# Optimization experiments

Measured on AMD Instinct MI355X. Metric: run time of the kernel, lower is better.

The kernel has to match this reference:

```python
import jax, jax.numpy as jnp
import numpy as np

B, NW, NS, SL = 32, 500, 50, 40
EMB, HID, VOCAB, E = 300, 150, 50000, 563200
N = B * (NW + NS)
MAXPOS = 512


def _sinusoid(n_pos, d):
    pos = np.arange(n_pos)[:, None].astype(np.float64)
    i = np.arange(d)[None, :]
    ang = pos / np.power(10000.0, 2 * (i // 2) / d)
    tab = np.zeros((n_pos, d))
    tab[:, 0::2] = np.sin(ang[:, 0::2])
    tab[:, 1::2] = np.cos(ang[:, 1::2])
    tab[0] = 0.0  # padding_idx=0
    return jnp.asarray(tab, dtype=jnp.float32)

_POS_TAB = _sinusoid(MAXPOS + 1, EMB)


def setup_inputs():
    keys = iter(jax.random.split(jax.random.key(0), 48))
    def nrm(shape, s=0.05):
        return jax.random.normal(next(keys), shape, dtype=jnp.float32) * s
    inp = {}
    inp["x"] = jax.random.randint(next(keys), (B, NW), 0, VOCAB, dtype=jnp.int32)
    inp["sent_x"] = jax.random.randint(next(keys), (B, NS, SL), 0, VOCAB, dtype=jnp.int32)
    inp["edge_index"] = jax.random.randint(next(keys), (2, E), 0, N, dtype=jnp.int32)
    inp["embed_table"] = nrm((VOCAB, EMB)).at[0].set(0.0)  # padding_idx=0
    for h in range(2, 8):
        inp["conv_w%d" % h] = nrm((50, 1, h, EMB))
        inp["conv_b%d" % h] = nrm((50,))
    inp["cnn_proj_w"] = nrm((HID, EMB)); inp["cnn_proj_b"] = nrm((HID,))
    inp["lstm_w_ih_l0"] = nrm((2, 4 * HID, HID)); inp["lstm_w_hh_l0"] = nrm((2, 4 * HID, HID))
    inp["lstm_b_ih_l0"] = nrm((2, 4 * HID)); inp["lstm_b_hh_l0"] = nrm((2, 4 * HID))
    inp["lstm_w_ih_l1"] = nrm((2, 4 * HID, 2 * HID)); inp["lstm_w_hh_l1"] = nrm((2, 4 * HID, HID))
    inp["lstm_b_ih_l1"] = nrm((2, 4 * HID)); inp["lstm_b_hh_l1"] = nrm((2, 4 * HID))
    inp["lstm_proj_w"] = nrm((HID, 2 * HID)); inp["lstm_proj_b"] = nrm((HID,))
    inp["gc0_w"] = nrm((HID, EMB)); inp["gc0_b"] = nrm((HID,))
    inp["gc1_w"] = nrm((HID, HID)); inp["gc1_b"] = nrm((HID,))
    inp["gc2_w"] = nrm((HID, HID)); inp["gc2_b"] = nrm((HID,))
    return inp


def _forward(x, sent_x, edge_index, embed_table, conv_ws, conv_bs,
             cnn_proj_w, cnn_proj_b, w_ih0, w_hh0, b_ih0, b_hh0,
             w_ih1, w_hh1, b_ih1, b_hh1, lstm_proj_w, lstm_proj_b,
             gc0_w, gc0_b, gc1_w, gc1_b, gc2_w, gc2_b):
    Bsz, S, L = sent_x.shape
    Nn = Bsz * S
    emb_words = embed_table[x]                                   # [B, NW, EMB]
    tok = embed_table[sent_x].reshape(Nn, L, EMB)                # [Nn, L, EMB]
    sentlen = (sent_x != 0).sum(-1).reshape(Nn)                  # token count per sentence
    a = jnp.arange(L)
    input_pos = jnp.where(a[None, :] < sentlen[:, None], a[None, :] + 1, 0)
    enc = tok + _POS_TAB[input_pos]
    # CNN ngram features: conv heights 2..7, full-width kernels == windowed matmuls
    feats = []
    for w, b in zip(conv_ws, conv_bs):
        h = w.shape[2]
        acc = b + sum(jnp.einsum('nld,od->nlo', enc[:, k:L - h + 1 + k, :], w[:, 0, k, :]) for k in range(h))
        feats.append(jnp.max(jax.nn.relu(acc), axis=1))          # [Nn, 50]
    ngram = jnp.concatenate(feats, axis=1)                        # [Nn, 300]
    snode_pos = jnp.tile(jnp.arange(S), Bsz)
    cnn_feat = ((ngram + _POS_TAB[snode_pos]) @ cnn_proj_w.T + cnn_proj_b).reshape(Bsz, S, HID)
    glen = (sent_x[:, :, 0] != 0).sum(-1)                         # valid sentence count per graph

    def lstm_dir(xs, w_ih, w_hh, bias):
        def step(carry, xt):
            hh, cc = carry
            g = xt @ w_ih.T + hh @ w_hh.T + bias
            i, f, gg, o = jnp.split(g, 4, axis=-1)
            cc = jax.nn.sigmoid(f) * cc + jax.nn.sigmoid(i) * jnp.tanh(gg)
            hh = jax.nn.sigmoid(o) * jnp.tanh(cc)
            return (hh, cc), hh
        z = jnp.zeros((xs.shape[0], HID), xs.dtype)
        _, hs = jax.lax.scan(step, (z, z), jnp.swapaxes(xs, 0, 1))
        return jnp.swapaxes(hs, 0, 1)

    def rev_within(xs):
        # reverse only the first glen[b] steps (packed-sequence semantics)
        T = xs.shape[1]; t = jnp.arange(T)
        idx = jnp.where(t[None, :] < glen[:, None], glen[:, None] - 1 - t[None, :], t[None, :])
        return jnp.take_along_axis(xs, idx[:, :, None], axis=1)

    def bidir(xs, w_ih, w_hh, b_i, b_h):
        f = lstm_dir(xs, w_ih[0], w_hh[0], b_i[0] + b_h[0])
        r = rev_within(lstm_dir(rev_within(xs), w_ih[1], w_hh[1], b_i[1] + b_h[1]))
        return jnp.concatenate([f, r], axis=-1)

    h1 = bidir(cnn_feat, w_ih0, w_hh0, b_ih0, b_hh0)
    h2 = bidir(h1, w_ih1, w_hh1, b_ih1, b_hh1)
    mask = (jnp.arange(S)[None, :] < glen[:, None]).astype(h2.dtype)[:, :, None]
    lstm_feat = (h2 * mask) @ lstm_proj_w.T + lstm_proj_b
    sent_out = jnp.concatenate([cnn_feat, lstm_feat], axis=-1)    # [B, S, 300]
    nodes = jnp.concatenate([emb_words, sent_out], axis=1)        # [B, NW+S, 300]
    nodes = (nodes @ gc0_w.T + gc0_b).reshape(-1, HID)            # [N, 150]
    Nt = nodes.shape[0]
    loop = jnp.arange(Nt, dtype=edge_index.dtype)
    src = jnp.concatenate([edge_index[0], loop])                  # add self-loops
    dst = jnp.concatenate([edge_index[1], loop])
    deg = jax.ops.segment_sum(jnp.ones(src.shape[0], nodes.dtype), dst, num_segments=Nt)
    dis = jnp.where(deg > 0, jax.lax.rsqrt(deg), 0.0)
    norm = (dis[src] * dis[dst])[:, None]

    def gcn(xin, w, bias):
        xw = xin @ w.T
        return jax.ops.segment_sum(xw[src] * norm, dst, num_segments=Nt) + bias

    h = jax.nn.elu(gcn(nodes, gc1_w, gc1_b))
    # F.dropout with training=False -> identity
    return gcn(h, gc2_w, gc2_b), emb_words


def reference(x, sent_x, edge_index, embed_table, conv_w2, conv_b2, conv_w3, conv_b3,
              conv_w4, conv_b4, conv_w5, conv_b5, conv_w6, conv_b6, conv_w7, conv_b7,
              cnn_proj_w, cnn_proj_b, lstm_w_ih_l0, lstm_w_hh_l0, lstm_b_ih_l0, lstm_b_hh_l0,
              lstm_w_ih_l1, lstm_w_hh_l1, lstm_b_ih_l1, lstm_b_hh_l1, lstm_proj_w, lstm_proj_b,
              gc0_w, gc0_b, gc1_w, gc1_b, gc2_w, gc2_b):
    conv_ws = [conv_w2, conv_w3, conv_w4, conv_w5, conv_w6, conv_w7]
    conv_bs = [conv_b2, conv_b3, conv_b4, conv_b5, conv_b6, conv_b7]
    return _forward(x, sent_x, edge_index, embed_table, conv_ws, conv_bs,
                    cnn_proj_w, cnn_proj_b, lstm_w_ih_l0, lstm_w_hh_l0, lstm_b_ih_l0, lstm_b_hh_l0,
                    lstm_w_ih_l1, lstm_w_hh_l1, lstm_b_ih_l1, lstm_b_hh_l1, lstm_proj_w, lstm_proj_b,
                    gc0_w, gc0_b, gc1_w, gc1_b, gc2_w, gc2_b)
```

## Files before the change

kernel.cpp:

```cpp
#include <hip/hip_runtime.h>
#include <stdint.h>
#include <math.h>

#define EDGES 563200
#define NNODES 17600
#define OUT0SZ 2640000
#define MROWS 64000
#define MPAD  64016
#define KSTRIDE 2112

typedef _Float16 h2 __attribute__((ext_vector_type(2)));
typedef _Float16 h4 __attribute__((ext_vector_type(4)));
typedef _Float16 v8h __attribute__((ext_vector_type(8)));
typedef float v4f __attribute__((ext_vector_type(4)));

__device__ __forceinline__ float sigm(float x){ return 1.f / (1.f + expf(-x)); }

__device__ __forceinline__ float fdot2_(h2 a, h2 b, float c){
#if __has_builtin(__builtin_amdgcn_fdot2)
  return __builtin_amdgcn_fdot2(a, b, c, false);
#else
  return c + (float)a.x * (float)b.x + (float)a.y * (float)b.y;
#endif
}

__device__ __forceinline__ void stage16(const char* g, char* lds_base, int lane){
#if __has_builtin(__builtin_amdgcn_global_load_lds)
  __builtin_amdgcn_global_load_lds(
      (const __attribute__((address_space(1))) void*)g,
      (__attribute__((address_space(3))) void*)lds_base, 16, 0, 0);
#else
  uint4 v = *(const uint4*)g;
  *(uint4*)(lds_base + lane * 16) = v;
#endif
}

__global__ __launch_bounds__(1024)
void gcnk_prep2(const int* __restrict__ sx, int* __restrict__ sentlen,
                int* __restrict__ glen_g, int* __restrict__ rowmap){
  __shared__ int sg[32];
  int tid = threadIdx.x;
  for (int i = tid; i < 1600; i += 1024){
    int c = 0;
    for (int j = 0; j < 40; j++) c += (sx[i * 40 + j] != 0);
    sentlen[i] = c;
  }
  if (tid < 32){
    int c = 0;
    for (int s = 0; s < 50; s++) c += (sx[tid * 2000 + s * 40] != 0);
    glen_g[tid] = c; sg[tid] = c;
  }
  __syncthreads();
  for (int i = tid; i < 1600; i += 1024){
    int b = i / 50, t = i - b * 50, g = sg[b];
    rowmap[i] = b * 50 + ((t < g) ? (g - 1 - t) : t);
  }
}

__global__ __launch_bounds__(256)
void gcnk_mergedprep(float* __restrict__ pos,
                     const float* w2, const float* w3, const float* w4,
                     const float* w5, const float* w6, const float* w7,
                     const float* c2, const float* c3, const float* c4,
                     const float* c5, const float* c6, const float* c7,
                     _Float16* __restrict__ Bp, float* __restrict__ bias_p,
                     const float* __restrict__ whh0, _Float16* __restrict__ wpad0,
                     const float* __restrict__ whh1, _Float16* __restrict__ wpad1,
                     unsigned int* __restrict__ ngram_u, unsigned int* __restrict__ ecnt_u,
                     const int* __restrict__ x, const float* __restrict__ tab,
                     float4* __restrict__ out1){
  int blk = blockIdx.x, tid = threadIdx.x;
  if (blk < 602){
    int idx = blk * 256 + tid;
    if (idx >= 513 * 300) return;
    int p = idx / 300, i = idx - p * 300;
    float v = 0.f;
    if (p != 0){
      double expo = (double)(2 * (i / 2)) / 300.0;
      double ang = (double)p / pow(10000.0, expo);
      v = (float)((i & 1) ? cos(ang) : sin(ang));
    }
    pos[idx] = v;
  } else if (blk < 3242){
    int idx = (blk - 602) * 256 + tid;
    if (idx < 2 * 160 * KSTRIDE){
      int n = idx / KSTRIDE, kk = idx - n * KSTRIDE;
      int g = n / 160, c = n - g * 160;
      _Float16 v = (_Float16)0.f;
      if (c < 150){
        int H = 3 * g + 2 + c / 50, o = c % 50;
        if (kk < 300 * H){
          const float* w;
          switch (H){ case 2: w = w2; break; case 3: w = w3; break;
                      case 4: w = w4; break; case 5: w = w5; break;
                      case 6: w = w6; break; default: w = w7; break; }
          v = (_Float16)w[o * 300 * H + kk];
        }
      }
      Bp[idx] = v;
    }
    if (idx < 320){
      int g = idx / 160, c = idx - g * 160;
      float bv = 0.f;
      if (c < 150){
        int H = 3 * g + 2 + c / 50, o = c % 50;
        const float* cbp;
        switch (H){ case 2: cbp = c2; break; case 3: cbp = c3; break;
                    case 4: cbp = c4; break; case 5: cbp = c5; break;
                    case 6: cbp = c6; break; default: cbp = c7; break; }
        bv = cbp[o];
      }
      bias_p[idx] = bv;
    }
  } else if (blk < 3955){
    int idx = (blk - 3242) * 256 + tid;
    if (idx >= 1200 * 152) return;
    int row = idx / 152, col = idx - row * 152;
    wpad0[idx] = (col < 150) ? (_Float16)whh0[row * 150 + col] : (_Float16)0.f;
  } else if (blk < 4668){
    int idx = (blk - 3955) * 256 + tid;
    if (idx >= 1200 * 152) return;
    int row = idx / 152, col = idx - row * 152;
    wpad1[idx] = (col < 150) ? (_Float16)whh1[row * 150 + col] : (_Float16)0.f;
  } else if (blk < 6543){
    int idx = (blk - 4668) * 256 + tid;
    if (idx < 1600 * 300) ngram_u[idx] = 0u;
  } else if (blk < 6612){
    int idx = (blk - 6543) * 256 + tid;
    if (idx < NNODES) ecnt_u[idx] = 0u;
  } else {
    int idx = (blk - 6612) * 256 + tid;
    if (idx >= 16000 * 75) return;
    int row = idx / 75, q = idx - row * 75;
    const float4* t = (const float4*)tab;
    out1[idx] = t[x[row] * 75 + q];
  }
}

__global__ void gcnk_ench(const int* __restrict__ sx, const float* __restrict__ tab,
                          const float* __restrict__ pos, const int* __restrict__ sentlen,
                          _Float16* __restrict__ ench){
  int idx = blockIdx.x * 256 + threadIdx.x;
  if (idx >= MPAD * 75) return;
  int row = idx / 75, q = idx - row * 75;
  int d = q * 4;
  h4 o; o[0] = (_Float16)0.f; o[1] = (_Float16)0.f; o[2] = (_Float16)0.f; o[3] = (_Float16)0.f;
  if (row < MROWS){
    int n = row / 40, l = row - n * 40;
    int tok = sx[n * 40 + l];
    int p = (l < sentlen[n]) ? (l + 1) : 0;
    float4 a = *(const float4*)(tab + (size_t)tok * 300 + d);
    float4 b = *(const float4*)(pos + (size_t)p * 300 + d);
    o[0] = (_Float16)(a.x + b.x); o[1] = (_Float16)(a.y + b.y);
    o[2] = (_Float16)(a.z + b.z); o[3] = (_Float16)(a.w + b.w);
  }
  *(h4*)(ench + (size_t)row * 300 + d) = o;
}

__global__ __launch_bounds__(256)
void gcnk_convmfma(const _Float16* __restrict__ A, const _Float16* __restrict__ Bp,
                   const float* __restrict__ bias_p, unsigned int* __restrict__ ngram_u){
  __shared__ __align__(1024) char smem[36864];
  _Float16* Asm = (_Float16*)smem;
  _Float16* Bsm = (_Float16*)(smem + 16384);
  float* Cs = (float*)smem;
  const int tid = threadIdx.x;
  const int m0 = blockIdx.x * 128;
  const int grp = blockIdx.y;
  const char* Abase = (const char*)A;
  const char* Bbase = (const char*)(Bp + (size_t)grp * 160 * KSTRIDE);
  const int kmax = grp ? 2112 : 1216;
  const int w = tid >> 6, lane = tid & 63;
  const int wm = (w >> 1) * 64, wn = (w & 1) * 80;
  const int fm = lane & 15, fq = lane >> 4;
  const int lrow = lane >> 3;
  const int loff = (((lane & 7) ^ lrow) << 4);

  v4f acc[4][5] = {};

  for (int kc = 0; kc < kmax; kc += 64){
    #pragma unroll
    for (int ii = 0; ii < 4; ii++){
      int i = w * 4 + ii;
      const char* g = Abase + (size_t)(m0 + i * 8 + lrow) * 600 + kc * 2 + loff;
      stage16(g, (char*)Asm + i * 1024, lane);
    }
    #pragma unroll
    for (int jj = 0; jj < 5; jj++){
      int j = w * 5 + jj;
      const char* g = Bbase + (size_t)(j * 8 + lrow) * (KSTRIDE * 2) + kc * 2 + loff;
      stage16(g, (char*)Bsm + j * 1024, lane);
    }
    __syncthreads();
    #pragma unroll
    for (int ks = 0; ks < 2; ks++){
      const int axor = (ks * 64 + fq * 16) ^ ((fm & 7) << 4);
      v8h af[4], bf[5];
      #pragma unroll
      for (int mt = 0; mt < 4; mt++)
        af[mt] = *(const v8h*)((const char*)Asm + (wm + mt * 16 + fm) * 128 + axor);
      #pragma unroll
      for (int nt = 0; nt < 5; nt++)
        bf[nt] = *(const v8h*)((const char*)Bsm + (wn + nt * 16 + fm) * 128 + axor);
      #pragma unroll
      for (int mt = 0; mt < 4; mt++)
        #pragma unroll
        for (int nt = 0; nt < 5; nt++)
          acc[mt][nt] = __builtin_amdgcn_mfma_f32_16x16x32_f16(af[mt], bf[nt], acc[mt][nt], 0, 0, 0);
    }
    __syncthreads();
  }

  for (int p = 0; p < 5; p++){
    __syncthreads();
    #pragma unroll
    for (int nt = 0; nt < 5; nt++){
      int cstart = wn + nt * 16;
      if ((cstart >> 5) == p){
        int co = cstart - p * 32 + fm;
        #pragma unroll
        for (int mt = 0; mt < 4; mt++)
          #pragma unroll
          for (int r = 0; r < 4; r++)
            Cs[(wm + mt * 16 + fq * 4 + r) * 33 + co] = acc[mt][nt][r];
      }
    }
    __syncthreads();
    if (tid < 128){
      int cl = tid & 31, si = tid >> 5;
      int col = p * 32 + cl;
      if (col < 150){
        int H = 3 * grp + 2 + col / 50, lh = 41 - H;
        int sent = m0 / 40 + si;
        if (sent < 1600){
          int rlo = sent * 40; if (rlo < m0) rlo = m0;
          int rhi = sent * 40 + lh; if (rhi > m0 + 128) rhi = m0 + 128;
          if (rlo < rhi){
            float bv = bias_p[grp * 160 + col];
            float vmax = 0.f;
            for (int r = rlo; r < rhi; r++){
              float v = Cs[(r - m0) * 33 + cl] + bv;
              vmax = fmaxf(vmax, v);
            }
            atomicMax(ngram_u + sent * 300 + grp * 150 + col, __float_as_uint(vmax));
          }
        }
      }
    }
  }
}

template<int BM, int BN, int WMT, int WNT, int OUTH>
__global__ __launch_bounds__(256)
void gcnk_mgemm(const float* __restrict__ A, const float* __restrict__ Wt,
                const float* __restrict__ b1, const float* __restrict__ b2,
                void* __restrict__ Cv, int M, int N, int K){
  __shared__ __align__(16) _Float16 As[BM * 40];
  __shared__ __align__(16) _Float16 Bs[BN * 40];
  const int tid = threadIdx.x;
  const int m0 = blockIdx.x * BM, n0 = blockIdx.y * BN;
  const int w = tid >> 6, lane = tid & 63;
  const int wm = (w >> 1) * (WMT * 16), wn = (w & 1) * (WNT * 16);
  const int fm = lane & 15, fq = lane >> 4;
  v4f acc[WMT][WNT] = {};
  const int nch = (K + 31) >> 5;
  for (int ch = 0; ch < nch; ch++){
    int kc = ch * 32;
    #pragma unroll
    for (int j = 0; j < BM / 64; j++){
      int u = tid + 256 * j;
      int row = u >> 2, cb = (u & 3) * 8;
      int gm = m0 + row, gk = kc + cb;
      v8h vv;
      if (gm < M && gk + 8 <= K){
        const float2* p = (const float2*)(A + (size_t)gm * K + gk);
        float2 q0 = p[0], q1 = p[1], q2 = p[2], q3 = p[3];
        vv[0] = (_Float16)q0.x; vv[1] = (_Float16)q0.y;
        vv[2] = (_Float16)q1.x; vv[3] = (_Float16)q1.y;
        vv[4] = (_Float16)q2.x; vv[5] = (_Float16)q2.y;
        vv[6] = (_Float16)q3.x; vv[7] = (_Float16)q3.y;
      } else {
        #pragma unroll
        for (int e = 0; e < 8; e++)
          vv[e] = (gm < M && gk + e < K) ? (_Float16)A[(size_t)gm * K + gk + e] : (_Float16)0.f;
      }
      *(v8h*)(As + row * 40 + cb) = vv;
    }
    {
      int row = tid >> 2, cb = (tid & 3) * 8;
      int gn = n0 + row, gk = kc + cb;
      v8h vv;
      if (gn < N && gk + 8 <= K){
        const float2* p = (const float2*)(Wt + (size_t)gn * K + gk);
        float2 q0 = p[0], q1 = p[1], q2 = p[2], q3 = p[3];
        vv[0] = (_Float16)q0.x; vv[1] = (_Float16)q0.y;
        vv[2] = (_Float16)q1.x; vv[3] = (_Float16)q1.y;
        vv[4] = (_Float16)q2.x; vv[5] = (_Float16)q2.y;
        vv[6] = (_Float16)q3.x; vv[7] = (_Float16)q3.y;
      } else {
        #pragma unroll
        for (int e = 0; e < 8; e++)
          vv[e] = (gn < N && gk + e < K) ? (_Float16)Wt[(size_t)gn * K + gk + e] : (_Float16)0.f;
      }
      *(v8h*)(Bs + row * 40 + cb) = vv;
    }
    __syncthreads();
    v8h af[WMT], bf[WNT];
    #pragma unroll
    for (int mt = 0; mt < WMT; mt++)
      af[mt] = *(const v8h*)(As + (wm + mt * 16 + fm) * 40 + fq * 8);
    #pragma unroll
    for (int nt = 0; nt < WNT; nt++)
      bf[nt] = *(const v8h*)(Bs + (wn + nt * 16 + fm) * 40 + fq * 8);
    #pragma unroll
    for (int mt = 0; mt < WMT; mt++)
      #pragma unroll
      for (int nt = 0; nt < WNT; nt++)
        acc[mt][nt] = __builtin_amdgcn_mfma_f32_16x16x32_f16(af[mt], bf[nt], acc[mt][nt], 0, 0, 0);
    __syncthreads();
  }
  #pragma unroll
  for (int nt = 0; nt < WNT; nt++){
    int gn = n0 + wn + nt * 16 + fm;
    if (gn >= N) continue;
    float badd = (b1 ? b1[gn] : 0.f) + (b2 ? b2[gn] : 0.f);
    #pragma unroll
    for (int mt = 0; mt < WMT; mt++)
      #pragma unroll
      for (int r = 0; r < 4; r++){
        int gm = m0 + wm + mt * 16 + fq * 4 + r;
        if (gm < M){
          float val = acc[mt][nt][r] + badd;
          if (OUTH) ((_Float16*)Cv)[(size_t)gm * 160 + gn] = (_Float16)val;
          else      ((float*)Cv)[(size_t)gm * N + gn] = val;
        }
      }
  }
}

__global__ __launch_bounds__(256)
void gcnk_mgemmH(const _Float16* __restrict__ Ah, const float* __restrict__ Wt,
                 const float* __restrict__ b1, float* __restrict__ C, int M, int N){
  const int K = 300;
  __shared__ __align__(16) _Float16 As[128 * 40];
  __shared__ __align__(16) _Float16 Bs[64 * 40];
  const int tid = threadIdx.x;
  const int m0 = blockIdx.x * 128, n0 = blockIdx.y * 64;
  const int w = tid >> 6, lane = tid & 63;
  const int wm = (w >> 1) * 64, wn = (w & 1) * 32;
  const int fm = lane & 15, fq = lane >> 4;
  v4f acc[4][2] = {};
  for (int ch = 0; ch < 10; ch++){
    int kc = ch * 32;
    #pragma unroll
    for (int j = 0; j < 2; j++){
      int u = tid + 256 * j;
      int row = u >> 2, cb = (u & 3) * 8;
      int gm = m0 + row, gk = kc + cb;
      v8h vv;
      if (gm < M && gk + 8 <= K){
        const char* p = (const char*)(Ah + (size_t)gm * 300 + gk);
        union { uint2 u2[2]; v8h v; } t;
        t.u2[0] = *(const uint2*)p; t.u2[1] = *(const uint2*)(p + 8);
        vv = t.v;
      } else {
        #pragma unroll
        for (int e = 0; e < 8; e++)
          vv[e] = (gm < M && gk + e < K) ? Ah[(size_t)gm * 300 + gk + e] : (_Float16)0.f;
      }
      *(v8h*)(As + row * 40 + cb) = vv;
    }
    {
      int row = tid >> 2, cb = (tid & 3) * 8;
      int gn = n0 + row, gk = kc + cb;
      v8h vv;
      if (gn < N && gk + 8 <= K){
        const float2* p = (const float2*)(Wt + (size_t)gn * K + gk);
        float2 q0 = p[0], q1 = p[1], q2 = p[2], q3 = p[3];
        vv[0] = (_Float16)q0.x; vv[1] = (_Float16)q0.y;
        vv[2] = (_Float16)q1.x; vv[3] = (_Float16)q1.y;
        vv[4] = (_Float16)q2.x; vv[5] = (_Float16)q2.y;
        vv[6] = (_Float16)q3.x; vv[7] = (_Float16)q3.y;
      } else {
        #pragma unroll
        for (int e = 0; e < 8; e++)
          vv[e] = (gn < N && gk + e < K) ? (_Float16)Wt[(size_t)gn * K + gk + e] : (_Float16)0.f;
      }
      *(v8h*)(Bs + row * 40 + cb) = vv;
    }
    __syncthreads();
    v8h af[4], bf[2];
    #pragma unroll
    for (int mt = 0; mt < 4; mt++)
      af[mt] = *(const v8h*)(As + (wm + mt * 16 + fm) * 40 + fq * 8);
    #pragma unroll
    for (int nt = 0; nt < 2; nt++)
      bf[nt] = *(const v8h*)(Bs + (wn + nt * 16 + fm) * 40 + fq * 8);
    #pragma unroll
    for (int mt = 0; mt < 4; mt++)
      #pragma unroll
      for (int nt = 0; nt < 2; nt++)
        acc[mt][nt] = __builtin_amdgcn_mfma_f32_16x16x32_f16(af[mt], bf[nt], acc[mt][nt], 0, 0, 0);
    __syncthreads();
  }
  #pragma unroll
  for (int nt = 0; nt < 2; nt++){
    int gn = n0 + wn + nt * 16 + fm;
    if (gn >= N) continue;
    float badd = b1[gn];
    #pragma unroll
    for (int mt = 0; mt < 4; mt++)
      #pragma unroll
      for (int r = 0; r < 4; r++){
        int gm = m0 + wm + mt * 16 + fq * 4 + r;
        if (gm < M) C[(size_t)gm * N + gn] = acc[mt][nt][r] + badd;
      }
  }
}

__global__ __launch_bounds__(256)
void gcnk_mgemmF(const float* __restrict__ A1, const int* __restrict__ mapA,
                 const float* __restrict__ A2, const int* __restrict__ mapB,
                 const int* __restrict__ glen, int usemask,
                 const float* __restrict__ apos,
                 const float* __restrict__ Wt, const float* __restrict__ b1,
                 const float* __restrict__ b2, float* __restrict__ C,
                 int M, int N, int K){
  const int BM = 64, WMT = 2, WNT = 2;
  __shared__ __align__(16) _Float16 As[BM * 40];
  __shared__ __align__(16) _Float16 Bs[64 * 40];
  const int tid = threadIdx.x;
  const int m0 = blockIdx.x * BM, n0 = blockIdx.y * 64;
  const int w = tid >> 6, lane = tid & 63;
  const int wm = (w >> 1) * (WMT * 16), wn = (w & 1) * (WNT * 16);
  const int fm = lane & 15, fq = lane >> 4;
  v4f acc[WMT][WNT] = {};
  const int nch = (K + 31) >> 5;
  for (int ch = 0; ch < nch; ch++){
    int kc = ch * 32;
    {
      int row = tid >> 2, cb = (tid & 3) * 8;
      int gm = m0 + row, gk = kc + cb;
      v8h vv;
      bool ok = (gm < M);
      if (ok && usemask){
        int b = gm / 50;
        if (gm - b * 50 >= glen[b]) ok = false;
      }
      if (!ok){
        #pragma unroll
        for (int e = 0; e < 8; e++) vv[e] = (_Float16)0.f;
      } else if (!A2){
        int r = mapA ? mapA[gm] : gm;
        const float* base = A1 + (size_t)r * K;
        if (gk + 8 <= K){
          const float2* p = (const float2*)(base + gk);
          float2 q0 = p[0], q1 = p[1], q2 = p[2], q3 = p[3];
          if (apos){
            const float2* a2 = (const float2*)(apos + (size_t)(gm % 50) * K + gk);
            float2 r0 = a2[0], r1 = a2[1], r2 = a2[2], r3 = a2[3];
            q0.x += r0.x; q0.y += r0.y; q1.x += r1.x; q1.y += r1.y;
            q2.x += r2.x; q2.y += r2.y; q3.x += r3.x; q3.y += r3.y;
          }
          vv[0] = (_Float16)q0.x; vv[1] = (_Float16)q0.y;
          vv[2] = (_Float16)q1.x; vv[3] = (_Float16)q1.y;
          vv[4] = (_Float16)q2.x; vv[5] = (_Float16)q2.y;
          vv[6] = (_Float16)q3.x; vv[7] = (_Float16)q3.y;
        } else {
          #pragma unroll
          for (int e = 0; e < 8; e++){
            int c = gk + e;
            float vf = (c < K) ? base[c] : 0.f;
            if (apos && c < K) vf += apos[(size_t)(gm % 50) * K + c];
            vv[e] = (_Float16)vf;
          }
        }
      } else {
        int rA = mapA ? mapA[gm] : gm;
        int rB = mapB ? mapB[gm] : gm;
        const float* pa = A1 + (size_t)rA * 150;
        const float* pb = A2 + (size_t)rB * 150;
        if (gk + 8 <= 150){
          const float2* p = (const float2*)(pa + gk);
          float2 q0 = p[0], q1 = p[1], q2 = p[2], q3 = p[3];
          vv[0] = (_Float16)q0.x; vv[1] = (_Float16)q0.y;
          vv[2] = (_Float16)q1.x; vv[3] = (_Float16)q1.y;
          vv[4] = (_Float16)q2.x; vv[5] = (_Float16)q2.y;
          vv[6] = (_Float16)q3.x; vv[7] = (_Float16)q3.y;
        } else if (gk >= 152 && gk + 8 <= K){
          const float2* p = (const float2*)(pb + gk - 150);
          float2 q0 = p[0], q1 = p[1], q2 = p[2], q3 = p[3];
          vv[0] = (_Float16)q0.x; vv[1] = (_Float16)q0.y;
          vv[2] = (_Float16)q1.x; vv[3] = (_Float16)q1.y;
          vv[4] = (_Float16)q2.x; vv[5] = (_Float16)q2.y;
          vv[6] = (_Float16)q3.x; vv[7] = (_Float16)q3.y;
        } else {
          #pragma unroll
          for (int e = 0; e < 8; e++){
            int c = gk + e;
            vv[e] = (c < 150) ? (_Float16)pa[c]
                  : ((c < K) ? (_Float16)pb[c - 150] : (_Float16)0.f);
          }
        }
      }
      *(v8h*)(As + row * 40 + cb) = vv;
    }
    {
      int row = tid >> 2, cb = (tid & 3) * 8;
      int gn = n0 + row, gk = kc + cb;
      v8h vv;
      if (gn < N && gk + 8 <= K){
        const float2* p = (const float2*)(Wt + (size_t)gn * K + gk);
        float2 q0 = p[0], q1 = p[1], q2 = p[2], q3 = p[3];
        vv[0] = (_Float16)q0.x; vv[1] = (_Float16)q0.y;
        vv[2] = (_Float16)q1.x; vv[3] = (_Float16)q1.y;
        vv[4] = (_Float16)q2.x; vv[5] = (_Float16)q2.y;
        vv[6] = (_Float16)q3.x; vv[7] = (_Float16)q3.y;
      } else {
        #pragma unroll
        for (int e = 0; e < 8; e++)
          vv[e] = (gn < N && gk + e < K) ? (_Float16)Wt[(size_t)gn * K + gk + e] : (_Float16)0.f;
      }
      *(v8h*)(Bs + row * 40 + cb) = vv;
    }
    __syncthreads();
    v8h af[WMT], bf[WNT];
    #pragma unroll
    for (int mt = 0; mt < WMT; mt++)
      af[mt] = *(const v8h*)(As + (wm + mt * 16 + fm) * 40 + fq * 8);
    #pragma unroll
    for (int nt = 0; nt < WNT; nt++)
      bf[nt] = *(const v8h*)(Bs + (wn + nt * 16 + fm) * 40 + fq * 8);
    #pragma unroll
    for (int mt = 0; mt < WMT; mt++)
      #pragma unroll
      for (int nt = 0; nt < WNT; nt++)
        acc[mt][nt] = __builtin_amdgcn_mfma_f32_16x16x32_f16(af[mt], bf[nt], acc[mt][nt], 0, 0, 0);
    __syncthreads();
  }
  #pragma unroll
  for (int nt = 0; nt < WNT; nt++){
    int gn = n0 + wn + nt * 16 + fm;
    if (gn >= N) continue;
    float badd = (b1 ? b1[gn] : 0.f) + (b2 ? b2[gn] : 0.f);
    #pragma unroll
    for (int mt = 0; mt < WMT; mt++)
      #pragma unroll
      for (int r = 0; r < 4; r++){
        int gm = m0 + wm + mt * 16 + fq * 4 + r;
        if (gm < M) C[(size_t)gm * N + gn] = acc[mt][nt][r] + badd;
      }
  }
}

struct FArgs {
  const float* A1; const int* mapA;
  const float* A2; const int* mapB;
  const float* Wt; const float* b1; const float* b2;
  float* C;
};

__global__ __launch_bounds__(256)
void gcnk_mgemmF2(FArgs pa, FArgs pb, int M, int N, int K){
  const int BM = 64, WMT = 2, WNT = 2;
  __shared__ __align__(16) _Float16 As[BM * 40];
  __shared__ __align__(16) _Float16 Bs[64 * 40];
  const FArgs P = blockIdx.z ? pb : pa;
  const int tid = threadIdx.x;
  const int m0 = blockIdx.x * BM, n0 = blockIdx.y * 64;
  const int w = tid >> 6, lane = tid & 63;
  const int wm = (w >> 1) * (WMT * 16), wn = (w & 1) * (WNT * 16);
  const int fm = lane & 15, fq = lane >> 4;
  v4f acc[WMT][WNT] = {};
  const int nch = (K + 31) >> 5;
  for (int ch = 0; ch < nch; ch++){
    int kc = ch * 32;
    {
      int row = tid >> 2, cb = (tid & 3) * 8;
      int gm = m0 + row, gk = kc + cb;
      v8h vv;
      if (gm >= M){
        #pragma unroll
        for (int e = 0; e < 8; e++) vv[e] = (_Float16)0.f;
      } else if (!P.A2){
        int r = P.mapA ? P.mapA[gm] : gm;
        const float* base = P.A1 + (size_t)r * K;
        if (gk + 8 <= K){
          const float2* p = (const float2*)(base + gk);
          float2 q0 = p[0], q1 = p[1], q2 = p[2], q3 = p[3];
          vv[0] = (_Float16)q0.x; vv[1] = (_Float16)q0.y;
          vv[2] = (_Float16)q1.x; vv[3] = (_Float16)q1.y;
          vv[4] = (_Float16)q2.x; vv[5] = (_Float16)q2.y;
          vv[6] = (_Float16)q3.x; vv[7] = (_Float16)q3.y;
        } else {
          #pragma unroll
          for (int e = 0; e < 8; e++)
            vv[e] = (gk + e < K) ? (_Float16)base[gk + e] : (_Float16)0.f;
        }
      } else {
        int rA = P.mapA ? P.mapA[gm] : gm;
        int rB = P.mapB ? P.mapB[gm] : gm;
        const float* paa = P.A1 + (size_t)rA * 150;
        const float* pbb = P.A2 + (size_t)rB * 150;
        if (gk + 8 <= 150){
          const float2* p = (const float2*)(paa + gk);
          float2 q0 = p[0], q1 = p[1], q2 = p[2], q3 = p[3];
          vv[0] = (_Float16)q0.x; vv[1] = (_Float16)q0.y;
          vv[2] = (_Float16)q1.x; vv[3] = (_Float16)q1.y;
          vv[4] = (_Float16)q2.x; vv[5] = (_Float16)q2.y;
          vv[6] = (_Float16)q3.x; vv[7] = (_Float16)q3.y;
        } else if (gk >= 152 && gk + 8 <= K){
          const float2* p = (const float2*)(pbb + gk - 150);
          float2 q0 = p[0], q1 = p[1], q2 = p[2], q3 = p[3];
          vv[0] = (_Float16)q0.x; vv[1] = (_Float16)q0.y;
          vv[2] = (_Float16)q1.x; vv[3] = (_Float16)q1.y;
          vv[4] = (_Float16)q2.x; vv[5] = (_Float16)q2.y;
          vv[6] = (_Float16)q3.x; vv[7] = (_Float16)q3.y;
        } else {
          #pragma unroll
          for (int e = 0; e < 8; e++){
            int c = gk + e;
            vv[e] = (c < 150) ? (_Float16)paa[c]
                  : ((c < K) ? (_Float16)pbb[c - 150] : (_Float16)0.f);
          }
        }
      }
      *(v8h*)(As + row * 40 + cb) = vv;
    }
    {
      int row = tid >> 2, cb = (tid & 3) * 8;
      int gn = n0 + row, gk = kc + cb;
      v8h vv;
      if (gn < N && gk + 8 <= K){
        const float2* p = (const float2*)(P.Wt + (size_t)gn * K + gk);
        float2 q0 = p[0], q1 = p[1], q2 = p[2], q3 = p[3];
        vv[0] = (_Float16)q0.x; vv[1] = (_Float16)q0.y;
        vv[2] = (_Float16)q1.x; vv[3] = (_Float16)q1.y;
        vv[4] = (_Float16)q2.x; vv[5] = (_Float16)q2.y;
        vv[6] = (_Float16)q3.x; vv[7] = (_Float16)q3.y;
      } else {
        #pragma unroll
        for (int e = 0; e < 8; e++)
          vv[e] = (gn < N && gk + e < K) ? (_Float16)P.Wt[(size_t)gn * K + gk + e] : (_Float16)0.f;
      }
      *(v8h*)(Bs + row * 40 + cb) = vv;
    }
    __syncthreads();
    v8h af[WMT], bf[WNT];
    #pragma unroll
    for (int mt = 0; mt < WMT; mt++)
      af[mt] = *(const v8h*)(As + (wm + mt * 16 + fm) * 40 + fq * 8);
    #pragma unroll
    for (int nt = 0; nt < WNT; nt++)
      bf[nt] = *(const v8h*)(Bs + (wn + nt * 16 + fm) * 40 + fq * 8);
    #pragma unroll
    for (int mt = 0; mt < WMT; mt++)
      #pragma unroll
      for (int nt = 0; nt < WNT; nt++)
        acc[mt][nt] = __builtin_amdgcn_mfma_f32_16x16x32_f16(af[mt], bf[nt], acc[mt][nt], 0, 0, 0);
    __syncthreads();
  }
  #pragma unroll
  for (int nt = 0; nt < WNT; nt++){
    int gn = n0 + wn + nt * 16 + fm;
    if (gn >= N) continue;
    float badd = (P.b1 ? P.b1[gn] : 0.f) + (P.b2 ? P.b2[gn] : 0.f);
    #pragma unroll
    for (int mt = 0; mt < WMT; mt++)
      #pragma unroll
      for (int r = 0; r < 4; r++){
        int gm = m0 + wm + mt * 16 + fq * 4 + r;
        if (gm < M) P.C[(size_t)gm * N + gn] = acc[mt][nt][r] + badd;
      }
  }
}

__global__ void gcnk_nodes_in_h(const int* __restrict__ x, const float* __restrict__ tab,
                                const float* __restrict__ cnnf, const float* __restrict__ lstmf,
                                h2* __restrict__ out){
  int idx = blockIdx.x * 256 + threadIdx.x;
  if (idx >= NNODES * 150) return;
  int nrow = idx / 150, q = idx - nrow * 150;
  int d = q * 2;
  int b = nrow / 550, j = nrow - b * 550;
  float2 v;
  if (j < 500) v = *(const float2*)(tab + (size_t)x[b * 500 + j] * 300 + d);
  else {
    int r = b * 50 + (j - 500);
    if (d < 150) v = *(const float2*)(cnnf + (size_t)r * 150 + d);
    else         v = *(const float2*)(lstmf + (size_t)r * 150 + d - 150);
  }
  h2 o; o[0] = (_Float16)v.x; o[1] = (_Float16)v.y;
  out[idx] = o;
}

__global__ __launch_bounds__(640)
void gcnk_lstm(const float* __restrict__ xf, const float* __restrict__ xr,
               const _Float16* __restrict__ wpad, float* __restrict__ fo,
               float* __restrict__ ro){
  int b = blockIdx.x >> 1, dir = blockIdx.x & 1;
  const float* xih = dir ? xr : xf;
  float* out = dir ? ro : fo;
  __shared__ __align__(16) _Float16 hh[160];
  __shared__ float gates[600];
  const int tid = threadIdx.x;

  h2 w[76];
  if (tid < 600){
    const h2* wrow = (const h2*)(wpad + ((size_t)dir * 600 + tid) * 152);
    #pragma unroll
    for (int j = 0; j < 76; j++) w[j] = wrow[j];
  }
  for (int u = tid; u < 160; u += 640) hh[u] = (_Float16)0.f;
  float creg = 0.f;
  __syncthreads();

  for (int t = 0; t < 50; t++){
    if (tid < 600){
      float acc = xih[(b * 50 + t) * 600 + tid];
      float a0 = 0.f, a1 = 0.f, a2 = 0.f, a3 = 0.f;
      #pragma unroll
      for (int j = 0; j < 19; j++){
        union { float4 f; h2 h[4]; } u;
        u.f = *(const float4*)(hh + j * 8);
        a0 = fdot2_(w[4 * j + 0], u.h[0], a0);
        a1 = fdot2_(w[4 * j + 1], u.h[1], a1);
        a2 = fdot2_(w[4 * j + 2], u.h[2], a2);
        a3 = fdot2_(w[4 * j + 3], u.h[3], a3);
      }
      gates[tid] = acc + ((a0 + a1) + (a2 + a3));
    }
    __syncthreads();
    if (tid < 150){
      float ig = sigm(gates[tid]);
      float fg = sigm(gates[150 + tid]);
      float gg = tanhf(gates[300 + tid]);
      float og = sigm(gates[450 + tid]);
      creg = fg * creg + ig * gg;
      float hn = og * tanhf(creg);
      hh[tid] = (_Float16)hn;
      out[(b * 50 + t) * 150 + tid] = hn;
    }
    __syncthreads();
  }
}

__global__ void gcnk_hist(const int* __restrict__ ei, int* __restrict__ ecnt){
  int e = blockIdx.x * 256 + threadIdx.x;
  if (e < EDGES) atomicAdd(&ecnt[ei[EDGES + e]], 1);
}

__global__ __launch_bounds__(1024)
void gcnk_scan(const int* __restrict__ ecnt, int* __restrict__ eoff,
               int* __restrict__ ecur, float* __restrict__ dis){
  __shared__ int wsum[16];
  int tid = threadIdx.x;
  int base = tid * 18;
  int pre[18];
  int s = 0;
  #pragma unroll
  for (int i = 0; i < 18; i++){
    int idx = base + i;
    int c = (idx < NNODES) ? ecnt[idx] : 0;
    if (idx < NNODES) dis[idx] = rsqrtf((float)(c + 1));
    pre[i] = s; s += c;
  }
  int lane = tid & 63, wid = tid >> 6;
  int run = s;
  #pragma unroll
  for (int off = 1; off < 64; off <<= 1){
    int y = __shfl_up(run, off, 64);
    if (lane >= off) run += y;
  }
  if (lane == 63) wsum[wid] = run;
  __syncthreads();
  if (tid == 0){
    int a = 0;
    #pragma unroll
    for (int i = 0; i < 16; i++){ int t2 = wsum[i]; wsum[i] = a; a += t2; }
  }
  __syncthreads();
  int excl = wsum[wid] + run - s;
  #pragma unroll
  for (int i = 0; i < 18; i++){
    int idx = base + i;
    if (idx < NNODES){
      int e = excl + pre[i];
      eoff[idx] = e; ecur[idx] = e;
    }
  }
}

__global__ void gcnk_scatter(const int* __restrict__ ei, int* __restrict__ ecur,
                             int* __restrict__ esrc){
  int e = blockIdx.x * 256 + threadIdx.x;
  if (e < EDGES){
    int d = ei[EDGES + e];
    int p = atomicAdd(&ecur[d], 1);
    esrc[p] = ei[e];
  }
}

__global__ __launch_bounds__(128)
void gcnk_aggcsr_h(const int* __restrict__ eoff, const int* __restrict__ ecnt,
                   const int* __restrict__ esrc, const float* __restrict__ dis,
                   const _Float16* __restrict__ xw, const float* __restrict__ bias,
                   float* __restrict__ out, int doelu){
  int d = blockIdx.x, t = threadIdx.x;
  float dd = dis[d];
  bool act = t < 75;
  float ax0 = 0.f, ay0 = 0.f, ax1 = 0.f, ay1 = 0.f;
  if (act){
    h2 v = *(const h2*)(xw + (size_t)d * 160 + 2 * t);
    ax0 = (float)v[0] * dd; ay0 = (float)v[1] * dd;
  }
  int beg = eoff[d], end = beg + ecnt[d];
  int j = beg;
  for (; j + 1 < end; j += 2){
    int s0 = esrc[j], s1 = esrc[j + 1];
    float d0 = dis[s0], d1 = dis[s1];
    if (act){
      h2 v0 = *(const h2*)(xw + (size_t)s0 * 160 + 2 * t);
      h2 v1 = *(const h2*)(xw + (size_t)s1 * 160 + 2 * t);
      ax0 += (float)v0[0] * d0; ay0 += (float)v0[1] * d0;
      ax1 += (float)v1[0] * d1; ay1 += (float)v1[1] * d1;
    }
  }
  if (j < end){
    int s = esrc[j];
    float ds_ = dis[s];
    if (act){
      h2 v = *(const h2*)(xw + (size_t)s * 160 + 2 * t);
      ax0 += (float)v[0] * ds_; ay0 += (float)v[1] * ds_;
    }
  }
  if (act){
    float o0 = (ax0 + ax1) * dd + bias[2 * t];
    float o1 = (ay0 + ay1) * dd + bias[2 * t + 1];
    if (doelu){
      o0 = (o0 > 0.f) ? o0 : expm1f(o0);
      o1 = (o1 > 0.f) ? o1 : expm1f(o1);
    }
    *(float2*)(out + (size_t)d * 150 + 2 * t) = make_float2(o0, o1);
  }
}

extern "C" void kernel_launch(void* const* d_in, const int* in_sizes, int n_in,
                              void* d_out, int out_size, void* d_ws, size_t ws_size,
                              hipStream_t stream){
  (void)in_sizes; (void)n_in; (void)out_size; (void)ws_size;

  char* wsb = (char*)d_ws;
  size_t off = 0;
  auto alloc = [&](size_t bytes) -> void* {
    void* p = wsb + off;
    off = (off + bytes + 255) & ~(size_t)255;
    return p;
  };
  float* pos_tab  = (float*)alloc(513 * 300 * 4);
  int*   sentlen  = (int*)alloc(1600 * 4);
  int*   glen     = (int*)alloc(32 * 4);
  int*   rowmap   = (int*)alloc(1600 * 4);
  float* ngram    = (float*)alloc(1600 * 300 * 4);
  float* cnn_feat = (float*)alloc(1600 * 150 * 4);
  float* xih_f    = (float*)alloc(1600 * 600 * 4);
  float* xih_r    = (float*)alloc(1600 * 600 * 4);
  float* f0       = (float*)alloc(1600 * 150 * 4);
  float* r0       = (float*)alloc(1600 * 150 * 4);
  float* f1       = (float*)alloc(1600 * 150 * 4);
  float* r1       = (float*)alloc(1600 * 150 * 4);
  float* lstm_ft  = (float*)alloc(1600 * 150 * 4);
  h2*    nodes_ih = (h2*)alloc((size_t)NNODES * 150 * 4);
  float* nodes    = (float*)alloc((size_t)NNODES * 150 * 4);
  float* dis      = (float*)alloc(NNODES * 4);
  _Float16* xwh   = (_Float16*)alloc((size_t)NNODES * 160 * 2);
  _Float16* ench  = (_Float16*)alloc((size_t)MPAD * 300 * 2);
  _Float16* Bp    = (_Float16*)alloc((size_t)2 * 160 * KSTRIDE * 2);
  float* bias_p   = (float*)alloc(320 * 4);
  _Float16* wpad0 = (_Float16*)alloc(1200 * 152 * 2);
  _Float16* wpad1 = (_Float16*)alloc(1200 * 152 * 2);
  int*   ecnt     = (int*)alloc(NNODES * 4);
  int*   eoff     = (int*)alloc(NNODES * 4);
  int*   ecur     = (int*)alloc(NNODES * 4);
  int*   esrc     = (int*)alloc(EDGES * 4);

  const int*   x   = (const int*)d_in[0];
  const int*   sx  = (const int*)d_in[1];
  const int*   ei  = (const int*)d_in[2];
  const float* tab = (const float*)d_in[3];
  const float *cw[6], *cb[6];
  for (int h = 0; h < 6; h++){ cw[h] = (const float*)d_in[4 + 2 * h]; cb[h] = (const float*)d_in[5 + 2 * h]; }
  const float* cnnw = (const float*)d_in[16]; const float* cnnb = (const float*)d_in[17];
  const float* wih0 = (const float*)d_in[18]; const float* whh0 = (const float*)d_in[19];
  const float* bih0 = (const float*)d_in[20]; const float* bhh0 = (const float*)d_in[21];
  const float* wih1 = (const float*)d_in[22]; const float* whh1 = (const float*)d_in[23];
  const float* bih1 = (const float*)d_in[24]; const float* bhh1 = (const float*)d_in[25];
  const float* lpw  = (const float*)d_in[26]; const float* lpb  = (const float*)d_in[27];
  const float* g0w  = (const float*)d_in[28]; const float* g0b  = (const float*)d_in[29];
  const float* g1w  = (const float*)d_in[30]; const float* g1b  = (const float*)d_in[31];
  const float* g2w  = (const float*)d_in[32]; const float* g2b  = (const float*)d_in[33];

  float* out0 = (float*)d_out;
  float4* out1 = (float4*)((float*)d_out + OUT0SZ);

  auto mgemmLH = [&](const float* A, const float* W, void* C, int M, int N, int K){
    dim3 g((M + 127) / 128, (N + 63) / 64);
    gcnk_mgemm<128, 64, 4, 2, 1><<<g, 256, 0, stream>>>(A, W, nullptr, nullptr, C, M, N, K);
  };
  auto mgemmF = [&](const float* A1, const int* mapA, const float* A2, const int* mapB,
                    const int* gl, int um, const float* apos, const float* W,
                    const float* b1, const float* b2, float* C, int N, int K){
    dim3 g(25, (N + 63) / 64);
    gcnk_mgemmF<<<g, 256, 0, stream>>>(A1, mapA, A2, mapB, gl, um, apos, W, b1, b2, C, 1600, N, K);
  };

  gcnk_prep2<<<1, 1024, 0, stream>>>(sx, sentlen, glen, rowmap);
  gcnk_mergedprep<<<11300, 256, 0, stream>>>(
      pos_tab, cw[0], cw[1], cw[2], cw[3], cw[4], cw[5],
      cb[0], cb[1], cb[2], cb[3], cb[4], cb[5], Bp, bias_p,
      whh0, wpad0, whh1, wpad1, (unsigned int*)ngram, (unsigned int*)ecnt,
      x, tab, out1);
  gcnk_ench<<<(MPAD * 75 + 255) / 256, 256, 0, stream>>>(sx, tab, pos_tab, sentlen, ench);

  {
    dim3 g(500, 2);
    gcnk_convmfma<<<g, 256, 0, stream>>>(ench, Bp, bias_p, (unsigned int*)ngram);
  }

  mgemmF(ngram, nullptr, nullptr, nullptr, nullptr, 0, pos_tab,
         cnnw, cnnb, nullptr, cnn_feat, 150, 300);

  {
    FArgs pa{cnn_feat, nullptr, nullptr, nullptr, wih0,             bih0,       bhh0,       xih_f};
    FArgs pb{cnn_feat, rowmap,  nullptr, nullptr, wih0 + 600 * 150, bih0 + 600, bhh0 + 600, xih_r};
    dim3 g(25, 10, 2);
    gcnk_mgemmF2<<<g, 256, 0, stream>>>(pa, pb, 1600, 600, 150);
  }
  gcnk_lstm<<<64, 640, 0, stream>>>(xih_f, xih_r, wpad0, f0, r0);

  {
    FArgs pa{f0, nullptr, r0, rowmap,  wih1,             bih1,       bhh1,       xih_f};
    FArgs pb{f0, rowmap,  r0, nullptr, wih1 + 600 * 300, bih1 + 600, bhh1 + 600, xih_r};
    dim3 g(25, 10, 2);
    gcnk_mgemmF2<<<g, 256, 0, stream>>>(pa, pb, 1600, 600, 300);
  }
  gcnk_lstm<<<64, 640, 0, stream>>>(xih_f, xih_r, wpad1, f1, r1);

  mgemmF(f1, nullptr, r1, rowmap, glen, 1, nullptr, lpw, lpb, nullptr, lstm_ft, 150, 300);

  gcnk_nodes_in_h<<<(NNODES * 150 + 255) / 256, 256, 0, stream>>>(x, tab, cnn_feat, lstm_ft, nodes_ih);
  {
    dim3 g(138, 3);
    gcnk_mgemmH<<<g, 256, 0, stream>>>((const _Float16*)nodes_ih, g0w, g0b, nodes, NNODES, 150);
  }

  gcnk_hist<<<2200, 256, 0, stream>>>(ei, ecnt);
  gcnk_scan<<<1, 1024, 0, stream>>>(ecnt, eoff, ecur, dis);
  gcnk_scatter<<<2200, 256, 0, stream>>>(ei, ecur, esrc);

  mgemmLH(nodes, g1w, xwh, NNODES, 150, 150);
  gcnk_aggcsr_h<<<NNODES, 128, 0, stream>>>(eoff, ecnt, esrc, dis, xwh, g1b, nodes, 1);

  mgemmLH(nodes, g2w, xwh, NNODES, 150, 150);
  gcnk_aggcsr_h<<<NNODES, 128, 0, stream>>>(eoff, ecnt, esrc, dis, xwh, g2b, out0, 0);
}
```

Baseline: 769.2 us.

## Double-buffer conv MFMA shared-memory tiles with smaller K chunks

Restructures the conv n-gram GEMM main loop to use two shared-memory buffers of 32-wide K chunks, so the next chunk is staged while MFMAs run on the current one. The loop now needs one barrier per chunk instead of two. The swizzle and staging layout are changed to fit 64-byte rows. In exchange it runs twice as many iterations with half the work each, and whether loads actually overlap depends on stage16 being asynchronous.

```diff
diff --git a/kernel.cpp b/kernel.cpp
--- a/kernel.cpp
+++ b/kernel.cpp
@@ -161,53 +161,59 @@
 void gcnk_convmfma(const _Float16* __restrict__ A, const _Float16* __restrict__ Bp,
                    const float* __restrict__ bias_p, unsigned int* __restrict__ ngram_u){
   __shared__ __align__(1024) char smem[36864];
-  _Float16* Asm = (_Float16*)smem;
-  _Float16* Bsm = (_Float16*)(smem + 16384);
   float* Cs = (float*)smem;
   const int tid = threadIdx.x;
   const int m0 = blockIdx.x * 128;
   const int grp = blockIdx.y;
   const char* Abase = (const char*)A;
   const char* Bbase = (const char*)(Bp + (size_t)grp * 160 * KSTRIDE);
-  const int kmax = grp ? 2112 : 1216;
+  const int nch = (grp ? 2112 : 1216) >> 5;
   const int w = tid >> 6, lane = tid & 63;
   const int wm = (w >> 1) * 64, wn = (w & 1) * 80;
   const int fm = lane & 15, fq = lane >> 4;
-  const int lrow = lane >> 3;
-  const int loff = (((lane & 7) ^ lrow) << 4);
+  const int lrow = lane >> 2;
+  const int sslot = (((lane & 3) ^ ((lane >> 3) & 3)) << 4);
 
   v4f acc[4][5] = {};
 
-  for (int kc = 0; kc < kmax; kc += 64){
-    #pragma unroll
-    for (int ii = 0; ii < 4; ii++){
-      int i = w * 4 + ii;
-      const char* g = Abase + (size_t)(m0 + i * 8 + lrow) * 600 + kc * 2 + loff;
-      stage16(g, (char*)Asm + i * 1024, lane);
-    }
-    #pragma unroll
-    for (int jj = 0; jj < 5; jj++){
-      int j = w * 5 + jj;
-      const char* g = Bbase + (size_t)(j * 8 + lrow) * (KSTRIDE * 2) + kc * 2 + loff;
-      stage16(g, (char*)Bsm + j * 1024, lane);
-    }
-    __syncthreads();
-    #pragma unroll
-    for (int ks = 0; ks < 2; ks++){
-      const int axor = (ks * 64 + fq * 16) ^ ((fm & 7) << 4);
-      v8h af[4], bf[5];
-      #pragma unroll
-      for (int mt = 0; mt < 4; mt++)
-        af[mt] = *(const v8h*)((const char*)Asm + (wm + mt * 16 + fm) * 128 + axor);
+  auto stageChunk = [&](int buf, int kc){
+    char* Asm = smem + buf * 18432;
+    char* Bsm = Asm + 8192;
+    #pragma unroll
+    for (int ii = 0; ii < 2; ii++){
+      int i = w * 2 + ii;
+      const char* g = Abase + (size_t)(m0 + i * 16 + lrow) * 600 + kc * 2 + sslot;
+      stage16(g, Asm + i * 1024, lane);
+    }
+    for (int j = w; j < 10; j += 4){
+      const char* g = Bbase + (size_t)(j * 16 + lrow) * (KSTRIDE * 2) + kc * 2 + sslot;
+      stage16(g, Bsm + j * 1024, lane);
+    }
+  };
+
+  stageChunk(0, 0);
+  __syncthreads();
+  for (int c = 0; c < nch; c++){
+    int cur = c & 1;
+    if (c + 1 < nch) stageChunk(cur ^ 1, (c + 1) * 32);
+    const char* Asm = smem + cur * 18432;
+    const char* Bsm = Asm + 8192;
+    v8h af[4], bf[5];
+    #pragma unroll
+    for (int mt = 0; mt < 4; mt++){
+      int r = wm + mt * 16 + fm;
+      af[mt] = *(const v8h*)(Asm + r * 64 + ((fq ^ ((r >> 1) & 3)) << 4));
+    }
+    #pragma unroll
+    for (int nt = 0; nt < 5; nt++){
+      int r = wn + nt * 16 + fm;
+      bf[nt] = *(const v8h*)(Bsm + r * 64 + ((fq ^ ((r >> 1) & 3)) << 4));
+    }
+    #pragma unroll
+    for (int mt = 0; mt < 4; mt++)
       #pragma unroll
       for (int nt = 0; nt < 5; nt++)
-        bf[nt] = *(const v8h*)((const char*)Bsm + (wn + nt * 16 + fm) * 128 + axor);
-      #pragma unroll
-      for (int mt = 0; mt < 4; mt++)
-        #pragma unroll
-        for (int nt = 0; nt < 5; nt++)
-          acc[mt][nt] = __builtin_amdgcn_mfma_f32_16x16x32_f16(af[mt], bf[nt], acc[mt][nt], 0, 0, 0);
-    }
+        acc[mt][nt] = __builtin_amdgcn_mfma_f32_16x16x32_f16(af[mt], bf[nt], acc[mt][nt], 0, 0, 0);
     __syncthreads();
   }
 
```

Result: no change. 774.6 us (+0.7%).
